# Kernel tuning notes

Hardware: AMD Instinct MI355X
Metric: run time of the kernel (lower is better)

## Reference

```python
import jax, jax.numpy as jnp
import numpy as np

N, E, D, H, C = 50000, 800000, 128, 2, 128
NEG_SLOPE = 0.2
EPS = 1e-16  # matches pyg softmax denominator epsilon


def _xavier(k, shape):
    fan_out, fan_in = shape[0], shape[-1]
    lim = float(np.sqrt(6.0 / (fan_in + fan_out)))
    return jax.random.uniform(k, shape, jnp.float32, -lim, lim)


def setup_inputs() -> dict:
    key = jax.random.key(0)
    ks = jax.random.split(key, 10)
    x = jax.random.normal(ks[0], (N, D), jnp.float32)
    edge_index = jax.random.randint(ks[1], (2, E), 0, N, dtype=jnp.int64)
    W1 = _xavier(ks[2], (H * C, D))
    att_l1 = _xavier(ks[3], (H, C))
    att_r1 = _xavier(ks[4], (H, C))
    W2 = _xavier(ks[5], (H * C, H * C))
    att_l2 = _xavier(ks[6], (H, C))
    att_r2 = _xavier(ks[7], (H, C))
    Wp1 = _xavier(ks[8], (C, H * C))
    bp1 = jnp.zeros((C,), jnp.float32)
    Wp2 = _xavier(ks[9], (C, C))
    bp2 = jnp.zeros((C,), jnp.float32)
    return dict(x=x, edge_index=edge_index, W1=W1, att_l1=att_l1, att_r1=att_r1,
                W2=W2, att_l2=att_l2, att_r2=att_r2, Wp1=Wp1, bp1=bp1, Wp2=Wp2, bp2=bp2)


def gat_layer(x, W, att_l, att_r, src, dst):
    n = x.shape[0]
    xl = (x @ W.T).reshape(n, H, C)              # lin_l == lin_r (shared)
    alpha_l = (xl * att_l).sum(-1)               # [n, H]
    alpha_r = (xl * att_r).sum(-1)               # [n, H]
    # per-edge attention logits: alpha_j (source) + alpha_i (dest)
    e = jax.nn.leaky_relu(alpha_l[src] + alpha_r[dst], NEG_SLOPE)  # [E, H]
    # segment softmax over incoming edges of each destination node
    m = jax.ops.segment_max(e, dst, num_segments=n)
    m = jnp.where(jnp.isfinite(m), m, 0.0)
    ex = jnp.exp(e - m[dst])
    denom = jax.ops.segment_sum(ex, dst, num_segments=n)
    a = ex / (denom[dst] + EPS)                  # [E, H]
    # weighted message + scatter-sum aggregation
    out = jax.ops.segment_sum(a[:, :, None] * xl[src], dst, num_segments=n)
    return out.reshape(n, H * C)


def reference(x, edge_index, W1, att_l1, att_r1, W2, att_l2, att_r2, Wp1, bp1, Wp2, bp2):
    src, dst = edge_index[0], edge_index[1]
    h = jax.nn.relu(gat_layer(x, W1, att_l1, att_r1, src, dst))   # dropout p=0 -> no-op
    h = jax.nn.relu(gat_layer(h, W2, att_l2, att_r2, src, dst))
    h = h @ Wp1.T + bp1
    h = h @ Wp2.T + bp2
    return h
```

## Files before the change

kernel.cpp:

```cpp
#include <hip/hip_runtime.h>
#include <hip/hip_bf16.h>
#include <stdint.h>

#define HC 256
#define NEG_SLOPE 0.2f
#define SOFTMAX_EPS 1e-16f
#define CSR_CAP 6144
#define PART_EPB 2048

typedef float floatx4 __attribute__((ext_vector_type(4)));
typedef _Float16 half8v __attribute__((ext_vector_type(8)));

__device__ __forceinline__ float in_load(const void* p, int i, int is_bf16) {
    return is_bf16 ? (float)((const __bf16*)p)[i] : ((const float*)p)[i];
}

__device__ __forceinline__ int edge_is64(const int* ei) {
    const uint32_t* ew = (const uint32_t*)ei;
    uint32_t myw = ew[2 * (threadIdx.x & 63) + 1];
    return (__ballot(myw != 0u) == 0ull) ? 1 : 0;
}
__device__ __forceinline__ int edge_src(const int* ei, int E, int e, int is64) {
    return is64 ? ei[2 * (size_t)e] : ei[e];
}
__device__ __forceinline__ int edge_dst(const int* ei, int E, int e, int is64) {
    return is64 ? ei[2 * (size_t)E + 2 * (size_t)e] : ei[(size_t)E + e];
}

__global__ void prep_partition_kernel(
    const void* __restrict__ xin, _Float16* __restrict__ x16, int nx,
    const void* __restrict__ w1,  _Float16* __restrict__ W1f, int n1,
    const void* __restrict__ w2,  _Float16* __restrict__ W2f, int n2,
    const void* __restrict__ wp1, _Float16* __restrict__ Wp1f, int n3,
    const void* __restrict__ wp2, _Float16* __restrict__ Wp2f, int n4,
    const void* __restrict__ a0, float* __restrict__ o0, int m0,
    const void* __restrict__ a1, float* __restrict__ o1, int m1,
    const void* __restrict__ a2, float* __restrict__ o2, int m2,
    const void* __restrict__ a3, float* __restrict__ o3, int m3,
    const void* __restrict__ a4, float* __restrict__ o4, int m4,
    const void* __restrict__ a5, float* __restrict__ o5, int m5,
    const int* __restrict__ ei, int E,
    int* __restrict__ bcnt, uint2* __restrict__ stage,
    int part_blocks) {
    if (blockIdx.x < part_blocks) {
        __shared__ int hist[256];
        __shared__ int chunk[256];
        __shared__ uint2 eLDS[PART_EPB];
        const int t = threadIdx.x;
        const int is64 = edge_is64(ei);
        const int ebase = blockIdx.x * PART_EPB;
        hist[t] = 0;
        __syncthreads();
        for (int i = t; i < PART_EPB; i += 256) {
            const int e = ebase + i;
            uint2 sd = make_uint2(0u, 0xFFFFFFFFu);
            if (e < E) {
                sd.x = (uint32_t)edge_src(ei, E, e, is64);
                sd.y = (uint32_t)edge_dst(ei, E, e, is64);
                atomicAdd(&hist[sd.y >> 8], 1);
            }
            eLDS[i] = sd;
        }
        __syncthreads();
        const int h = hist[t];
        if (h > 0) chunk[t] = atomicAdd(&bcnt[t * 16], h);
        __syncthreads();
        hist[t] = 0;
        __syncthreads();
        for (int i = t; i < PART_EPB; i += 256) {
            const uint2 sd = eLDS[i];
            if (sd.y != 0xFFFFFFFFu) {
                const int b = (int)(sd.y >> 8);
                const int local = atomicAdd(&hist[b], 1);
                const int pos = chunk[b] + local;
                if (pos < CSR_CAP)
                    stage[(size_t)b * CSR_CAP + pos] =
                        make_uint2(sd.x, sd.y & 255u);
            }
        }
        return;
    }
    const uint32_t w = ((const uint32_t*)xin)[threadIdx.x & 63];
    const uint32_t ef = ((w & 0xFFFFu) >> 7) & 0xFFu;
    const int fb = (__popcll(__ballot(ef >= 90u && ef <= 135u)) > 48) ? 1 : 0;

    int off = (blockIdx.x - part_blocks) * blockDim.x + threadIdx.x;
    if (off < nx) { x16[off] = (_Float16)in_load(xin, off, fb); return; }
    off -= nx;
    if (off < n1) { W1f[off] = (_Float16)in_load(w1, off, fb); return; }
    off -= n1;
    if (off < n2) { W2f[off] = (_Float16)in_load(w2, off, fb); return; }
    off -= n2;
    if (off < n3) { Wp1f[off] = (_Float16)in_load(wp1, off, fb); return; }
    off -= n3;
    if (off < n4) { Wp2f[off] = (_Float16)in_load(wp2, off, fb); return; }
    off -= n4;
    if (off < m0) { o0[off] = in_load(a0, off, fb); return; }
    off -= m0;
    if (off < m1) { o1[off] = in_load(a1, off, fb); return; }
    off -= m1;
    if (off < m2) { o2[off] = in_load(a2, off, fb); return; }
    off -= m2;
    if (off < m3) { o3[off] = in_load(a3, off, fb); return; }
    off -= m3;
    if (off < m4) { o4[off] = in_load(a4, off, fb); return; }
    off -= m4;
    if (off < m5) { o5[off] = in_load(a5, off, fb); return; }
}

__global__ __launch_bounds__(1024) void bucket_csr_kernel(
    const int* __restrict__ bcnt, const uint2* __restrict__ stage,
    int* __restrict__ row_ptr, int* __restrict__ esrc, int nb, int N) {
    __shared__ int scanv[256];
    __shared__ int hist[256];
    __shared__ int fill[256];
    __shared__ int wsum[4], wpre[4];
    const int b = blockIdx.x;
    const int t = threadIdx.x;
    const int lane = t & 63;
    const int wv = t >> 6;

    if (t < 256) {
        const int v = (t < nb) ? min(bcnt[t * 16], CSR_CAP) : 0;
        int inc = v;
#pragma unroll
        for (int off = 1; off < 64; off <<= 1) {
            int y = __shfl_up(inc, off);
            if (lane >= off) inc += y;
        }
        if (lane == 63) wsum[wv] = inc;
        __syncthreads();
        if (t == 0) {
            int run = 0;
#pragma unroll
            for (int ww = 0; ww < 4; ww++) { wpre[ww] = run; run += wsum[ww]; }
        }
        __syncthreads();
        const int excl = wpre[wv] + inc - v;
        scanv[t] = excl;
        if (b == 0 && t == nb - 1) row_ptr[N] = excl + v;
        hist[t] = 0;
    } else {
        __syncthreads();
        __syncthreads();
    }
    __syncthreads();

    const int base = scanv[b];
    const int cnt = min(bcnt[b * 16], CSR_CAP);
    const uint2* st = stage + (size_t)b * CSR_CAP;

    for (int i = t; i < cnt; i += 1024) atomicAdd(&hist[st[i].y], 1);
    __syncthreads();
    if (t < 256) {
        const int hv = hist[t];
        int hinc = hv;
#pragma unroll
        for (int off = 1; off < 64; off <<= 1) {
            int y = __shfl_up(hinc, off);
            if (lane >= off) hinc += y;
        }
        if (lane == 63) wsum[wv] = hinc;
        __syncthreads();
        if (t == 0) {
            int run = 0;
#pragma unroll
            for (int ww = 0; ww < 4; ww++) { wpre[ww] = run; run += wsum[ww]; }
        }
        __syncthreads();
        const int hexcl = wpre[wv] + hinc - hv;
        fill[t] = hexcl;
        const int node = (b << 8) + t;
        if (node < N) row_ptr[node] = base + hexcl;
    } else {
        __syncthreads();
        __syncthreads();
    }
    __syncthreads();
    for (int i = t; i < cnt; i += 1024) {
        const uint2 e = st[i];
        const int pos = atomicAdd(&fill[e.y], 1);
        esrc[base + pos] = (int)e.x;
    }
}

template <int KTEMP>
__global__ __launch_bounds__(256, 4) void gemm_alpha_kernel(
    const _Float16* __restrict__ A, const _Float16* __restrict__ B,
    _Float16* __restrict__ Cf16,
    const float* __restrict__ attl, const float* __restrict__ attr,
    float* __restrict__ al, float* __restrict__ ar,
    int M) {
    const int bx = blockIdx.x;
    const int head = bx & 1;
    const int mbase = (bx >> 1) * 64;
    const int tid = threadIdx.x;
    const int lane = tid & 63;
    const int wave = tid >> 6;
    const int l15 = lane & 15;
    const int q = lane >> 4;
    const int kq = q * 8;
    const int wc = head * 128 + wave * 32;

    int arow[4];
#pragma unroll
    for (int rt = 0; rt < 4; rt++) arow[rt] = min(mbase + rt * 16 + l15, M - 1);

    floatx4 acc[4][2];
#pragma unroll
    for (int rt = 0; rt < 4; rt++)
#pragma unroll
        for (int tt = 0; tt < 2; tt++) acc[rt][tt] = (floatx4){0.f, 0.f, 0.f, 0.f};

    constexpr int KSTEPS = KTEMP / 32;
#pragma unroll
    for (int ks = 0; ks < KSTEPS; ks++) {
        const int k0 = ks * 32;
        half8v af[4], bf[2];
#pragma unroll
        for (int rt = 0; rt < 4; rt++)
            af[rt] = *(const half8v*)(A + (size_t)arow[rt] * KTEMP + k0 + kq);
#pragma unroll
        for (int tt = 0; tt < 2; tt++)
            bf[tt] = *(const half8v*)(B + (size_t)(wc + tt * 16 + l15) * KTEMP + k0 + kq);
#pragma unroll
        for (int rt = 0; rt < 4; rt++)
#pragma unroll
            for (int tt = 0; tt < 2; tt++)
                acc[rt][tt] = __builtin_amdgcn_mfma_f32_16x16x32_f16(af[rt], bf[tt], acc[rt][tt], 0, 0, 0);
    }

    float aLp[4][4], aRp[4][4];
#pragma unroll
    for (int rt = 0; rt < 4; rt++)
#pragma unroll
        for (int r = 0; r < 4; r++) { aLp[rt][r] = 0.f; aRp[rt][r] = 0.f; }

#pragma unroll
    for (int rt = 0; rt < 4; rt++) {
        const int rb = mbase + rt * 16 + q * 4;
#pragma unroll
        for (int tt = 0; tt < 2; tt++) {
            const int gcol = wc + tt * 16 + l15;
            const float atlv = attl[gcol], atrv = attr[gcol];
#pragma unroll
            for (int r = 0; r < 4; r++) {
                const float v = acc[rt][tt][r];
                aLp[rt][r] += v * atlv;
                aRp[rt][r] += v * atrv;
                const int grow = rb + r;
                if (grow < M) Cf16[(size_t)grow * 256 + gcol] = (_Float16)v;
            }
        }
    }

    __shared__ float sAL[4][64], sAR[4][64];
#pragma unroll
    for (int rt = 0; rt < 4; rt++)
#pragma unroll
        for (int r = 0; r < 4; r++) {
            float vl = aLp[rt][r], vr = aRp[rt][r];
            vl += __shfl_xor(vl, 1); vl += __shfl_xor(vl, 2);
            vl += __shfl_xor(vl, 4); vl += __shfl_xor(vl, 8);
            vr += __shfl_xor(vr, 1); vr += __shfl_xor(vr, 2);
            vr += __shfl_xor(vr, 4); vr += __shfl_xor(vr, 8);
            if (l15 == 0) {
                sAL[wave][rt * 16 + q * 4 + r] = vl;
                sAR[wave][rt * 16 + q * 4 + r] = vr;
            }
        }
    __syncthreads();
    if (tid < 64) {
        const int grow = mbase + tid;
        if (grow < M) {
            al[2 * grow + head] = sAL[0][tid] + sAL[1][tid] + sAL[2][tid] + sAL[3][tid];
            ar[2 * grow + head] = sAR[0][tid] + sAR[1][tid] + sAR[2][tid] + sAR[3][tid];
        }
    }
}

__global__ __launch_bounds__(256, 2) void proj_fused_kernel(
    const _Float16* __restrict__ A, const _Float16* __restrict__ B1,
    const float* __restrict__ b1, const _Float16* __restrict__ B2,
    const float* __restrict__ b2, float* __restrict__ out, int M) {
    __shared__ _Float16 plds[64 * 128];
    const int tid = threadIdx.x;
    const int lane = tid & 63;
    const int wave = tid >> 6;
    const int mbase = blockIdx.x * 64;
    const int l15 = lane & 15;
    const int q = lane >> 4;
    const int kq = q * 8;
    const int wc = wave * 32;

    int arow[4];
#pragma unroll
    for (int rt = 0; rt < 4; rt++) arow[rt] = min(mbase + rt * 16 + l15, M - 1);

    floatx4 acc[4][2];
#pragma unroll
    for (int rt = 0; rt < 4; rt++)
#pragma unroll
        for (int tt = 0; tt < 2; tt++) acc[rt][tt] = (floatx4){0.f, 0.f, 0.f, 0.f};
#pragma unroll
    for (int ks = 0; ks < 8; ks++) {
        const int k0 = ks * 32;
        half8v af[4], bf[2];
#pragma unroll
        for (int rt = 0; rt < 4; rt++)
            af[rt] = *(const half8v*)(A + (size_t)arow[rt] * 256 + k0 + kq);
#pragma unroll
        for (int tt = 0; tt < 2; tt++)
            bf[tt] = *(const half8v*)(B1 + (size_t)(wc + tt * 16 + l15) * 256 + k0 + kq);
#pragma unroll
        for (int rt = 0; rt < 4; rt++)
#pragma unroll
            for (int tt = 0; tt < 2; tt++)
                acc[rt][tt] = __builtin_amdgcn_mfma_f32_16x16x32_f16(af[rt], bf[tt], acc[rt][tt], 0, 0, 0);
    }
#pragma unroll
    for (int rt = 0; rt < 4; rt++) {
#pragma unroll
        for (int tt = 0; tt < 2; tt++) {
            const int col = wc + tt * 16 + l15;
            const float bv = b1[col];
#pragma unroll
            for (int r = 0; r < 4; r++) {
                const int row = rt * 16 + q * 4 + r;
                const int byt = row * 256 + ((((col >> 3) ^ (row & 15)) << 4)) + (col & 7) * 2;
                *(_Float16*)((char*)plds + byt) = (_Float16)(acc[rt][tt][r] + bv);
            }
        }
    }
    __syncthreads();

    floatx4 acc2[4][2];
#pragma unroll
    for (int rt = 0; rt < 4; rt++)
#pragma unroll
        for (int tt = 0; tt < 2; tt++) acc2[rt][tt] = (floatx4){0.f, 0.f, 0.f, 0.f};
#pragma unroll
    for (int ks = 0; ks < 4; ks++) {
        half8v af[4], bf[2];
#pragma unroll
        for (int rt = 0; rt < 4; rt++) {
            const int row = rt * 16 + l15;
            const int byt = (row << 8) + (((ks * 4 + q) ^ l15) << 4);
            af[rt] = *(const half8v*)((const char*)plds + byt);
        }
#pragma unroll
        for (int tt = 0; tt < 2; tt++)
            bf[tt] = *(const half8v*)(B2 + (size_t)(wc + tt * 16 + l15) * 128 + ks * 32 + kq);
#pragma unroll
        for (int rt = 0; rt < 4; rt++)
#pragma unroll
            for (int tt = 0; tt < 2; tt++)
                acc2[rt][tt] = __builtin_amdgcn_mfma_f32_16x16x32_f16(af[rt], bf[tt], acc2[rt][tt], 0, 0, 0);
    }
#pragma unroll
    for (int rt = 0; rt < 4; rt++) {
        const int rb = mbase + rt * 16 + q * 4;
#pragma unroll
        for (int tt = 0; tt < 2; tt++) {
            const int gcol = wc + tt * 16 + l15;
            const float bv = b2[gcol];
#pragma unroll
            for (int r = 0; r < 4; r++) {
                const int grow = rb + r;
                if (grow < M) out[(size_t)grow * 128 + gcol] = acc2[rt][tt][r] + bv;
            }
        }
    }
}

__global__ __launch_bounds__(256) void agg_fused_kernel(
    const _Float16* __restrict__ xl,
    const float* __restrict__ al, const float* __restrict__ ar,
    const int* __restrict__ row_ptr, const int* __restrict__ esrc,
    _Float16* __restrict__ hout, int N) {
    const int wid = (blockIdx.x * 256 + threadIdx.x) >> 6;
    if (wid >= N) return;
    const int lane = threadIdx.x & 63;
    const int half = lane >> 5;
    const int c8 = (lane & 31) * 8;
    const int hsel = c8 >> 7;
    const int hshift = hsel << 4;
    const int s0 = row_ptr[wid], e0 = row_ptr[wid + 1];
    const float ar0 = ar[2 * wid], ar1 = ar[2 * wid + 1];

    float acc[8];
#pragma unroll
    for (int c = 0; c < 8; c++) acc[c] = 0.f;
    float l0 = 0.f, l1 = 0.f;

    for (int base = s0; base < e0; base += 64) {
        const int n = min(64, e0 - base);
        int s = 0;
        float p0 = 0.f, p1 = 0.f;
        if (lane < n) {
            s = esrc[base + lane];
            float2 av = *(const float2*)(al + 2 * s);
            float lg0 = av.x + ar0; lg0 = lg0 > 0.f ? lg0 : NEG_SLOPE * lg0;
            float lg1 = av.y + ar1; lg1 = lg1 > 0.f ? lg1 : NEG_SLOPE * lg1;
            p0 = __expf(__builtin_fminf(lg0, 10.f));
            p1 = __expf(__builtin_fminf(lg1, 10.f));
        }
        auto pk2 = __builtin_amdgcn_cvt_pkrtz(p0, p1);
        const uint32_t pku = __builtin_bit_cast(uint32_t, pk2);
        l0 += (float)pk2[0];
        l1 += (float)pk2[1];

#pragma unroll 8
        for (int j = 0; j < n; j += 2) {
            const int jj = j + half;
            const uint32_t w32 = (uint32_t)__shfl((int)pku, jj);
            const int ss = __shfl(s, jj);
            const unsigned short wb = (unsigned short)(w32 >> hshift);
            const float wf = (float)__builtin_bit_cast(_Float16, wb);
            half8v xv = *(const half8v*)(xl + (size_t)ss * HC + c8);
#pragma unroll
            for (int c = 0; c < 8; c++) acc[c] += wf * (float)xv[c];
        }
    }

#pragma unroll
    for (int off = 1; off < 64; off <<= 1) {
        l0 += __shfl_xor(l0, off);
        l1 += __shfl_xor(l1, off);
    }
    const float winv = 1.f / ((hsel ? l1 : l0) + SOFTMAX_EPS);

#pragma unroll
    for (int c = 0; c < 8; c++) {
        acc[c] += __shfl_xor(acc[c], 32);
        acc[c] = fmaxf(acc[c] * winv, 0.f);
    }
    if (half == 0) {
        half8v vo;
#pragma unroll
        for (int c = 0; c < 8; c++) vo[c] = (_Float16)acc[c];
        *(half8v*)(hout + (size_t)wid * HC + c8) = vo;
    }
}

extern "C" void kernel_launch(void* const* d_in, const int* in_sizes, int n_in,
                              void* d_out, int out_size, void* d_ws, size_t ws_size,
                              hipStream_t stream) {
    const int D = 128;
    const int N = in_sizes[0] / D;
    const int E = in_sizes[1] / 2;
    const int* ei = (const int*)d_in[1];
    const int NBUCK = (N + 255) >> 8;

    char* w = (char*)d_ws;
    auto alloc = [&](size_t bytes) {
        void* p = w;
        w += (bytes + 255) & ~(size_t)255;
        return p;
    };
    _Float16* x16    = (_Float16*)alloc((size_t)N * D * 2);
    _Float16* W1f    = (_Float16*)alloc((size_t)in_sizes[2] * 2);
    _Float16* W2f    = (_Float16*)alloc((size_t)in_sizes[5] * 2);
    _Float16* Wp1f   = (_Float16*)alloc((size_t)in_sizes[8] * 2);
    _Float16* Wp2f   = (_Float16*)alloc((size_t)in_sizes[10] * 2);
    float*    atl1   = (float*)   alloc((size_t)in_sizes[3] * 4);
    float*    atr1   = (float*)   alloc((size_t)in_sizes[4] * 4);
    float*    atl2   = (float*)   alloc((size_t)in_sizes[6] * 4);
    float*    atr2   = (float*)   alloc((size_t)in_sizes[7] * 4);
    float*    bfp1   = (float*)   alloc((size_t)in_sizes[9] * 4);
    float*    bfp2   = (float*)   alloc((size_t)in_sizes[11] * 4);
    _Float16* xl16   = (_Float16*)alloc((size_t)N * HC * 2);
    _Float16* h16    = (_Float16*)alloc((size_t)N * HC * 2);
    float*    al     = (float*)   alloc((size_t)N * 2 * 4);
    float*    ar     = (float*)   alloc((size_t)N * 2 * 4);
    int*      row_ptr= (int*)     alloc((size_t)(N + 1) * 4);
    int*      esrc   = (int*)     alloc((size_t)E * 4);
    int*      bcnt   = (int*)     alloc((size_t)NBUCK * 16 * 4);
    uint2*    stage  = (uint2*)   alloc((size_t)NBUCK * CSR_CAP * 8);

    const int GM = (N + 63) / 64;
    const int AGG_B = (N + 3) / 4;
    const int PART_B = (E + PART_EPB - 1) / PART_EPB;

    (void)hipMemsetAsync(bcnt, 0, (size_t)NBUCK * 16 * 4, stream);
    {
        int ntot = in_sizes[0] + in_sizes[2] + in_sizes[5] + in_sizes[8] + in_sizes[10]
                 + in_sizes[3] + in_sizes[4] + in_sizes[6] + in_sizes[7]
                 + in_sizes[9] + in_sizes[11];
        int prep_blocks = (ntot + 255) / 256;
        prep_partition_kernel<<<PART_B + prep_blocks, 256, 0, stream>>>(
            d_in[0], x16, in_sizes[0],
            d_in[2], W1f, in_sizes[2],
            d_in[5], W2f, in_sizes[5],
            d_in[8], Wp1f, in_sizes[8],
            d_in[10], Wp2f, in_sizes[10],
            d_in[3], atl1, in_sizes[3],
            d_in[4], atr1, in_sizes[4],
            d_in[6], atl2, in_sizes[6],
            d_in[7], atr2, in_sizes[7],
            d_in[9], bfp1, in_sizes[9],
            d_in[11], bfp2, in_sizes[11],
            ei, E, bcnt, stage, PART_B);
    }

    bucket_csr_kernel<<<NBUCK, 1024, 0, stream>>>(bcnt, stage, row_ptr, esrc, NBUCK, N);

    gemm_alpha_kernel<128><<<2 * GM, 256, 0, stream>>>(
        x16, W1f, xl16, atl1, atr1, al, ar, N);
    agg_fused_kernel<<<AGG_B, 256, 0, stream>>>(xl16, al, ar, row_ptr, esrc, h16, N);

    gemm_alpha_kernel<256><<<2 * GM, 256, 0, stream>>>(
        h16, W2f, xl16, atl2, atr2, al, ar, N);
    agg_fused_kernel<<<AGG_B, 256, 0, stream>>>(xl16, al, ar, row_ptr, esrc, h16, N);

    proj_fused_kernel<<<GM, 256, 0, stream>>>(
        h16, Wp1f, bfp1, Wp2f, bfp2, (float*)d_out, N);
}
```

Before: 344.7 us.

## Stage GEMM A tiles into LDS via direct global-to-LDS loads

The GEMM-alpha and projection kernels now copy the 64-row A tile into shared memory with global_load_lds using an XOR swizzle, then read MFMA fragments from LDS instead of each wave reloading A from global memory. This removes the four-fold redundant global reads of A across waves. The cost is extra LDS per block, which may reduce occupancy, plus a barrier before compute. Separately, the partition kernel drops its LDS edge buffer and rereads edge indices from global memory in the second pass.

Result: faster. 329.6 us (-4.4%).

```diff
diff --git a/kernel.cpp b/kernel.cpp
--- a/kernel.cpp
+++ b/kernel.cpp
@@ -25,6 +25,35 @@
 }
 __device__ __forceinline__ int edge_dst(const int* ei, int E, int e, int is64) {
     return is64 ? ei[2 * (size_t)E + 2 * (size_t)e] : ei[(size_t)E + e];
+}
+
+template <int KT>
+__device__ __forceinline__ void stage_A(const _Float16* __restrict__ A,
+                                        int mbase, int M, _Float16* lds) {
+    constexpr int CH = KT / 8;
+    constexpr int ISSUES = (64 * CH) / 256;
+    const int w = threadIdx.x >> 6;
+    const int lane = threadIdx.x & 63;
+#pragma unroll
+    for (int i = 0; i < ISSUES; i++) {
+        const int j = i * 256 + w * 64 + lane;
+        const int row = j / CH;
+        const int chS = j % CH;
+        const int grow = min(mbase + row, M - 1);
+        const void* src = (const char*)A +
+            ((size_t)grow * KT + (size_t)(chS ^ (row & 15)) * 8) * 2;
+        void* dst = (char*)lds + (size_t)(i * 256 + w * 64) * 16;
+        __builtin_amdgcn_global_load_lds(src, dst, 16, 0, 0);
+    }
+}
+
+template <int KT>
+__device__ __forceinline__ half8v read_A(const _Float16* lds, int rt, int l15,
+                                         int ks, int q) {
+    constexpr int CH = KT / 8;
+    const int row = rt * 16 + l15;
+    const int slot = row * CH + ((ks * 4 + q) ^ (row & 15));
+    return *(const half8v*)(lds + (size_t)slot * 8);
 }
 
 __global__ void prep_partition_kernel(
@@ -45,7 +74,6 @@
     if (blockIdx.x < part_blocks) {
         __shared__ int hist[256];
         __shared__ int chunk[256];
-        __shared__ uint2 eLDS[PART_EPB];
         const int t = threadIdx.x;
         const int is64 = edge_is64(ei);
         const int ebase = blockIdx.x * PART_EPB;
@@ -53,13 +81,7 @@
         __syncthreads();
         for (int i = t; i < PART_EPB; i += 256) {
             const int e = ebase + i;
-            uint2 sd = make_uint2(0u, 0xFFFFFFFFu);
-            if (e < E) {
-                sd.x = (uint32_t)edge_src(ei, E, e, is64);
-                sd.y = (uint32_t)edge_dst(ei, E, e, is64);
-                atomicAdd(&hist[sd.y >> 8], 1);
-            }
-            eLDS[i] = sd;
+            if (e < E) atomicAdd(&hist[edge_dst(ei, E, e, is64) >> 8], 1);
         }
         __syncthreads();
         const int h = hist[t];
@@ -68,14 +90,16 @@
         hist[t] = 0;
         __syncthreads();
         for (int i = t; i < PART_EPB; i += 256) {
-            const uint2 sd = eLDS[i];
-            if (sd.y != 0xFFFFFFFFu) {
-                const int b = (int)(sd.y >> 8);
+            const int e = ebase + i;
+            if (e < E) {
+                const int s = edge_src(ei, E, e, is64);
+                const int d = edge_dst(ei, E, e, is64);
+                const int b = d >> 8;
                 const int local = atomicAdd(&hist[b], 1);
                 const int pos = chunk[b] + local;
                 if (pos < CSR_CAP)
                     stage[(size_t)b * CSR_CAP + pos] =
-                        make_uint2(sd.x, sd.y & 255u);
+                        make_uint2((uint32_t)s, (uint32_t)(d & 255));
             }
         }
         return;
@@ -191,6 +215,7 @@
     const float* __restrict__ attl, const float* __restrict__ attr,
     float* __restrict__ al, float* __restrict__ ar,
     int M) {
+    __shared__ _Float16 alds[64 * KTEMP];
     const int bx = blockIdx.x;
     const int head = bx & 1;
     const int mbase = (bx >> 1) * 64;
@@ -202,9 +227,8 @@
     const int kq = q * 8;
     const int wc = head * 128 + wave * 32;
 
-    int arow[4];
-#pragma unroll
-    for (int rt = 0; rt < 4; rt++) arow[rt] = min(mbase + rt * 16 + l15, M - 1);
+    stage_A<KTEMP>(A, mbase, M, alds);
+    __syncthreads();
 
     floatx4 acc[4][2];
 #pragma unroll
@@ -218,11 +242,11 @@
         const int k0 = ks * 32;
         half8v af[4], bf[2];
 #pragma unroll
-        for (int rt = 0; rt < 4; rt++)
-            af[rt] = *(const half8v*)(A + (size_t)arow[rt] * KTEMP + k0 + kq);
-#pragma unroll
         for (int tt = 0; tt < 2; tt++)
             bf[tt] = *(const half8v*)(B + (size_t)(wc + tt * 16 + l15) * KTEMP + k0 + kq);
+#pragma unroll
+        for (int rt = 0; rt < 4; rt++)
+            af[rt] = read_A<KTEMP>(alds, rt, l15, ks, q);
 #pragma unroll
         for (int rt = 0; rt < 4; rt++)
 #pragma unroll
@@ -283,6 +307,7 @@
     const _Float16* __restrict__ A, const _Float16* __restrict__ B1,
     const float* __restrict__ b1, const _Float16* __restrict__ B2,
     const float* __restrict__ b2, float* __restrict__ out, int M) {
+    __shared__ _Float16 alds[64 * 256];
     __shared__ _Float16 plds[64 * 128];
     const int tid = threadIdx.x;
     const int lane = tid & 63;
@@ -293,9 +318,8 @@
     const int kq = q * 8;
     const int wc = wave * 32;
 
-    int arow[4];
-#pragma unroll
-    for (int rt = 0; rt < 4; rt++) arow[rt] = min(mbase + rt * 16 + l15, M - 1);
+    stage_A<256>(A, mbase, M, alds);
+    __syncthreads();
 
     floatx4 acc[4][2];
 #pragma unroll
@@ -307,11 +331,11 @@
         const int k0 = ks * 32;
         half8v af[4], bf[2];
 #pragma unroll
-        for (int rt = 0; rt < 4; rt++)
-            af[rt] = *(const half8v*)(A + (size_t)arow[rt] * 256 + k0 + kq);
-#pragma unroll
         for (int tt = 0; tt < 2; tt++)
             bf[tt] = *(const half8v*)(B1 + (size_t)(wc + tt * 16 + l15) * 256 + k0 + kq);
+#pragma unroll
+        for (int rt = 0; rt < 4; rt++)
+            af[rt] = read_A<256>(alds, rt, l15, ks, q);
 #pragma unroll
         for (int rt = 0; rt < 4; rt++)
 #pragma unroll
```
